# Optimization experiments

Hardware: AMD Instinct MI355X
Metric: run time of the kernel (lower is better)

## Reference

```python
import jax, jax.numpy as jnp
import numpy as np

N = 8192      # nodes (N_features)
D = 64        # oscillator dimension
E_K = 262144  # Kuramoto coupling edges
E_HK = 262144 # Hopfield-Kuramoto coupling edges
H = 64        # interaction MLP hidden width (N_weights)
KAPPA_K = 2.0
KAPPA_H = 2.0


def setup_inputs() -> dict:
    key = jax.random.key(0)
    ks = jax.random.split(key, 9)
    return dict(
        state_H=jax.random.normal(ks[0], (N,), dtype=jnp.float32),
        state_K=jax.random.normal(ks[1], (N, D), dtype=jnp.float32),
        W_H=jax.random.normal(ks[2], (N, N), dtype=jnp.float32) / np.float32(np.sqrt(N)),
        omega=jax.random.normal(ks[3], (D, D), dtype=jnp.float32),
        w1=jax.random.normal(ks[4], (1, H), dtype=jnp.float32),
        b1=jnp.zeros((H,), dtype=jnp.float32),
        w2=jax.random.normal(ks[5], (H, 1), dtype=jnp.float32) / np.float32(np.sqrt(H)),
        ind_K=jax.random.randint(ks[6], (E_K, 2), 0, N),
        ind_HK=jax.random.randint(ks[7], (E_HK, 2), 0, N),
    )


def _interaction_K(s, w1, b1, w2):
    # edgewise scalar MLP: [E] -> [E], dE/ds of the Kuramoto interaction energy
    h = jnp.tanh(s[:, None] @ w1 + b1)  # [E, H]
    return (h @ w2)[:, 0]               # [E]


def reference(state_H, state_K, W_H, omega, w1, b1, w2, ind_K, ind_HK):
    # normalize oscillator states onto unit sphere (per node)
    state_K = state_K / jnp.linalg.norm(state_K, axis=1, keepdims=True)

    i, j = ind_HK[:, 0], ind_HK[:, 1]
    Gram = jnp.sum(state_K[i] * state_K[j], axis=1)  # [E_HK]

    # Hopfield model: g = LNet.get_g(state_H), f_H = Hopfield_model(t, state_H, ...)
    g = jnp.tanh(state_H)                 # [N]
    f_H = -state_H + W_H @ g              # [N] dense Hopfield dynamics
    f_H = f_H.at[i].add(Gram * g[j] / KAPPA_H)
    f_H = f_H.at[j].add(Gram * g[i] / KAPPA_H)

    # Kuramoto edge coupling
    p, q = ind_K[:, 0], ind_K[:, 1]
    s = jnp.sum(state_K[p] * state_K[q], axis=1)        # [E_K]
    dE_ds = _interaction_K(s, w1, b1, w2)[:, None]      # [E_K, 1]
    f_K = jnp.zeros_like(state_K)
    f_K = f_K.at[p].add(dE_ds * state_K[q])
    f_K = f_K.at[q].add(dE_ds * state_K[p])

    # Hopfield->Kuramoto coupling
    G = (g[i] * g[j])[:, None]                          # [E_HK, 1]
    f_K = f_K.at[i].add(-G * state_K[j] / KAPPA_K)
    f_K = f_K.at[j].add(-G * state_K[i] / KAPPA_K)

    # project onto tangent of the sphere + antisymmetric rotation
    f_K = (-f_K
           + state_K * jnp.sum(state_K * f_K, axis=1, keepdims=True)
           + state_K @ ((omega - omega.T) * 0.5))
    return (f_H, f_K)
```

## Files before the change

### kernel.cpp

```cpp
#include <hip/hip_runtime.h>
#include <math.h>

#define N 8192
#define D 64
#define E_K 262144
#define E_HK 262144
#define NEDGE (E_K + E_HK)
#define CAP 256

constexpr float INV_KAPPA = 0.5f;

__device__ inline float fast_tanh(float x) {
  x = fminf(15.f, fmaxf(-15.f, x));
  float e = __expf(2.f * x);
  return (e - 1.f) * __builtin_amdgcn_rcpf(e + 1.f);
}

__device__ inline float wave_reduce(float v) {
  #pragma unroll
  for (int off = 32; off > 0; off >>= 1) v += __shfl_xor(v, off);
  return v;
}

__global__ __launch_bounds__(256) void prep_scatter_kernel(
    const float* __restrict__ state_K, const float* __restrict__ state_H,
    const float* __restrict__ omega,
    const int* __restrict__ ind_HK, const int* __restrict__ ind_K,
    float* __restrict__ Knorm, float* __restrict__ g, float* __restrict__ Om,
    int* __restrict__ cursor, int* __restrict__ entries) {
  int b = blockIdx.x;
  if (b < 2048) {
    int t = b * 256 + threadIdx.x;
    int i, j, bit;
    if (t < E_HK) {
      int2 e = ((const int2*)ind_HK)[t];
      i = e.x; j = e.y; bit = (int)0x80000000;
    } else {
      int2 e = ((const int2*)ind_K)[t - E_HK];
      i = e.x; j = e.y; bit = 0;
    }
    int s0 = atomicAdd(&cursor[i], 1);
    if (s0 < CAP) entries[i * CAP + s0] = j | bit;
    int s1 = atomicAdd(&cursor[j], 1);
    if (s1 < CAP) entries[j * CAP + s1] = i | bit;
  } else if (b < 4096) {
    int lane = threadIdx.x & 63;
    int row  = (b - 2048) * 4 + (threadIdx.x >> 6);
    float v  = state_K[row * D + lane];
    float ss = wave_reduce(v * v);
    Knorm[row * D + lane] = v * __builtin_amdgcn_rcpf(sqrtf(ss));
    if (lane == 0) g[row] = fast_tanh(state_H[row]);
  } else {
    for (int t = threadIdx.x; t < D * D; t += 256) {
      int a = t >> 6, c = t & 63;
      Om[t] = 0.5f * (omega[a * D + c] - omega[c * D + a]);
    }
  }
}

__global__ __launch_bounds__(256) void mega_kernel(
    const float* __restrict__ W_H, const float* __restrict__ state_H,
    const float* __restrict__ Knorm, const float* __restrict__ g,
    const float* __restrict__ Om, const float* __restrict__ w1,
    const float* __restrict__ b1, const float* __restrict__ w2,
    const int* __restrict__ cursor, const int* __restrict__ entries,
    float* __restrict__ f_H, float* __restrict__ f_K) {
  int row  = blockIdx.x;
  int lane = threadIdx.x & 63;
  int wv   = threadIdx.x >> 6;

  const float4* Wrow = reinterpret_cast<const float4*>(W_H + (size_t)row * N);
  float4 wreg[8];
  #pragma unroll
  for (int k = 0; k < 8; ++k) wreg[k] = Wrow[threadIdx.x + k * 256];

  float kr  = Knorm[row * D + lane];
  float gr  = g[row];
  float w1l = w1[lane], b1l = b1[lane], w2l = w2[lane];

  __shared__ int sh_ent[CAP];
  int len = min(cursor[row], CAP);
  for (int e = threadIdx.x; e < len; e += 256)
    sh_ent[e] = entries[row * CAP + e];
  __syncthreads();

  float acc  = 0.f;
  float accH = 0.f;
  for (int e = wv; e < len; e += 4) {
    int ent   = sh_ent[e];
    int other = ent & 0x7FFFFFFF;
    float ko  = Knorm[other * D + lane];
    if (ent < 0) {
      float go = g[other];
      acc  += (-gr * go * INV_KAPPA) * ko;
      accH += go * ko;
    } else {
      float dot = wave_reduce(kr * ko);
      float de  = wave_reduce(fast_tanh(dot * w1l + b1l) * w2l);
      acc += de * ko;
    }
  }

  const float4* g4 = reinterpret_cast<const float4*>(g);
  float mv = 0.f;
  #pragma unroll
  for (int k = 0; k < 8; ++k) {
    float4 gg = g4[threadIdx.x + k * 256];
    mv += wreg[k].x * gg.x + wreg[k].y * gg.y +
          wreg[k].z * gg.z + wreg[k].w * gg.w;
  }
  mv = wave_reduce(mv);

  __shared__ float sAcc[4][D];
  __shared__ float sAccH[4][D];
  __shared__ float sMv[4];
  sAcc[wv][lane]  = acc;
  sAccH[wv][lane] = accH;
  if (lane == 0) sMv[wv] = mv;
  __syncthreads();

  if (wv == 0) {
    float tot  = sAcc[0][lane] + sAcc[1][lane] + sAcc[2][lane] + sAcc[3][lane];
    float totH = sAccH[0][lane] + sAccH[1][lane] + sAccH[2][lane] + sAccH[3][lane];
    float rd = wave_reduce(kr * tot);
    float sh = wave_reduce(kr * totH);
    float krot = 0.f;
    #pragma unroll
    for (int d = 0; d < D; ++d)
      krot += __shfl(kr, d) * Om[d * D + lane];
    f_K[row * D + lane] = -tot + kr * rd + krot;
    if (lane == 0)
      f_H[row] = -state_H[row] + sMv[0] + sMv[1] + sMv[2] + sMv[3]
                 + sh * INV_KAPPA;
  }
}

extern "C" void kernel_launch(void* const* d_in, const int* in_sizes, int n_in,
                              void* d_out, int out_size, void* d_ws, size_t ws_size,
                              hipStream_t stream) {
  const float* state_H = (const float*)d_in[0];
  const float* state_K = (const float*)d_in[1];
  const float* W_H     = (const float*)d_in[2];
  const float* omega   = (const float*)d_in[3];
  const float* w1      = (const float*)d_in[4];
  const float* b1      = (const float*)d_in[5];
  const float* w2      = (const float*)d_in[6];
  const int*   ind_K   = (const int*)d_in[7];
  const int*   ind_HK  = (const int*)d_in[8];

  float* f_H = (float*)d_out;
  float* f_K = (float*)d_out + N;

  char* ws = (char*)d_ws;
  int*   entries = (int*)ws;               ws += (size_t)N * CAP * sizeof(int);
  float* Knorm   = (float*)ws;             ws += (size_t)N * D * sizeof(float);
  float* g       = (float*)ws;             ws += N * sizeof(float);
  float* Om      = (float*)ws;             ws += D * D * sizeof(float);
  int*   cursor  = (int*)ws;

  hipMemsetAsync(cursor, 0, N * sizeof(int), stream);
  prep_scatter_kernel<<<4097, 256, 0, stream>>>(
      state_K, state_H, omega, ind_HK, ind_K, Knorm, g, Om, cursor, entries);
  mega_kernel<<<N, 256, 0, stream>>>(W_H, state_H, Knorm, g, Om, w1, b1, w2,
                                     cursor, entries, f_H, f_K);
}
```

Before: 499.2 us.

## Replace per-edge MLP with interpolated lookup table and batch edge dot reductions

Precomputes the scalar interaction MLP on a 2049-point grid over [-1,1] in the prep kernel and replaces the per-edge tanh MLP plus wave reduction with linear interpolation from a shared-memory table. Edge processing is also batched eight at a time so the neighbor loads and the shuffle reductions of the dot products are interleaved for more memory- and instruction-level parallelism. This removes one wave reduction and a tanh per Kuramoto edge, at the cost of interpolation error in the MLP output. Each block must also load the table into LDS, and register pressure goes up.

```diff
diff --git a/kernel.cpp b/kernel.cpp
--- a/kernel.cpp
+++ b/kernel.cpp
@@ -7,6 +7,8 @@
 #define E_HK 262144
 #define NEDGE (E_K + E_HK)
 #define CAP 256
+#define TAB_N 2048
+#define BATCH 8
 
 constexpr float INV_KAPPA = 0.5f;
 
@@ -26,8 +28,11 @@
     const float* __restrict__ state_K, const float* __restrict__ state_H,
     const float* __restrict__ omega,
     const int* __restrict__ ind_HK, const int* __restrict__ ind_K,
+    const float* __restrict__ w1, const float* __restrict__ b1,
+    const float* __restrict__ w2,
     float* __restrict__ Knorm, float* __restrict__ g, float* __restrict__ Om,
-    int* __restrict__ cursor, int* __restrict__ entries) {
+    float* __restrict__ Tab, int* __restrict__ cursor,
+    int* __restrict__ entries) {
   int b = blockIdx.x;
   if (b < 2048) {
     int t = b * 256 + threadIdx.x;
@@ -50,19 +55,27 @@
     float ss = wave_reduce(v * v);
     Knorm[row * D + lane] = v * __builtin_amdgcn_rcpf(sqrtf(ss));
     if (lane == 0) g[row] = fast_tanh(state_H[row]);
-  } else {
+  } else if (b == 4096) {
     for (int t = threadIdx.x; t < D * D; t += 256) {
       int a = t >> 6, c = t & 63;
       Om[t] = 0.5f * (omega[a * D + c] - omega[c * D + a]);
     }
+  } else {
+    int lane = threadIdx.x & 63;
+    int p = (b - 4097) * 4 + (threadIdx.x >> 6);
+    if (p <= TAB_N) {
+      float s = (float)p * (2.0f / TAB_N) - 1.0f;
+      float t = fast_tanh(s * w1[lane] + b1[lane]) * w2[lane];
+      t = wave_reduce(t);
+      if (lane == 0) Tab[p] = t;
+    }
   }
 }
 
 __global__ __launch_bounds__(256) void mega_kernel(
     const float* __restrict__ W_H, const float* __restrict__ state_H,
     const float* __restrict__ Knorm, const float* __restrict__ g,
-    const float* __restrict__ Om, const float* __restrict__ w1,
-    const float* __restrict__ b1, const float* __restrict__ w2,
+    const float* __restrict__ Om, const float* __restrict__ Tab,
     const int* __restrict__ cursor, const int* __restrict__ entries,
     float* __restrict__ f_H, float* __restrict__ f_K) {
   int row  = blockIdx.x;
@@ -74,30 +87,52 @@
   #pragma unroll
   for (int k = 0; k < 8; ++k) wreg[k] = Wrow[threadIdx.x + k * 256];
 
-  float kr  = Knorm[row * D + lane];
-  float gr  = g[row];
-  float w1l = w1[lane], b1l = b1[lane], w2l = w2[lane];
-
-  __shared__ int sh_ent[CAP];
+  float kr = Knorm[row * D + lane];
+  float gr = g[row];
+
+  __shared__ int   sh_ent[CAP];
+  __shared__ float sTab[TAB_N + 1];
   int len = min(cursor[row], CAP);
   for (int e = threadIdx.x; e < len; e += 256)
     sh_ent[e] = entries[row * CAP + e];
+  for (int t = threadIdx.x; t <= TAB_N; t += 256)
+    sTab[t] = Tab[t];
   __syncthreads();
 
   float acc  = 0.f;
   float accH = 0.f;
-  for (int e = wv; e < len; e += 4) {
-    int ent   = sh_ent[e];
-    int other = ent & 0x7FFFFFFF;
-    float ko  = Knorm[other * D + lane];
-    if (ent < 0) {
-      float go = g[other];
-      acc  += (-gr * go * INV_KAPPA) * ko;
-      accH += go * ko;
-    } else {
-      float dot = wave_reduce(kr * ko);
-      float de  = wave_reduce(fast_tanh(dot * w1l + b1l) * w2l);
-      acc += de * ko;
+  for (int base = wv * BATCH; base < len; base += 4 * BATCH) {
+    int   ents[BATCH];
+    float kov[BATCH], dv[BATCH];
+    #pragma unroll
+    for (int k = 0; k < BATCH; ++k) {
+      if (base + k < len) {
+        ents[k] = sh_ent[base + k];
+        kov[k]  = Knorm[(size_t)(ents[k] & 0x7FFFFFFF) * D + lane];
+      } else { ents[k] = 0; kov[k] = 0.f; }
+    }
+    #pragma unroll
+    for (int k = 0; k < BATCH; ++k) dv[k] = kr * kov[k];
+    #pragma unroll
+    for (int off = 32; off > 0; off >>= 1) {
+      #pragma unroll
+      for (int k = 0; k < BATCH; ++k) dv[k] += __shfl_xor(dv[k], off);
+    }
+    #pragma unroll
+    for (int k = 0; k < BATCH; ++k) {
+      int ent = ents[k];
+      if (ent < 0) {
+        float go = g[ent & 0x7FFFFFFF];
+        acc  += (-gr * go * INV_KAPPA) * kov[k];
+        accH += go * kov[k];
+      } else {
+        float x = fminf(fmaxf((dv[k] + 1.0f) * (TAB_N * 0.5f), 0.0f),
+                        (float)TAB_N);
+        int   i  = min((int)x, TAB_N - 1);
+        float fr = x - (float)i;
+        float de = sTab[i] + (sTab[i + 1] - sTab[i]) * fr;
+        acc += de * kov[k];
+      }
     }
   }
 
@@ -156,11 +191,13 @@
   float* Knorm   = (float*)ws;             ws += (size_t)N * D * sizeof(float);
   float* g       = (float*)ws;             ws += N * sizeof(float);
   float* Om      = (float*)ws;             ws += D * D * sizeof(float);
+  float* Tab     = (float*)ws;             ws += (TAB_N + 1) * sizeof(float);
   int*   cursor  = (int*)ws;
 
   hipMemsetAsync(cursor, 0, N * sizeof(int), stream);
-  prep_scatter_kernel<<<4097, 256, 0, stream>>>(
-      state_K, state_H, omega, ind_HK, ind_K, Knorm, g, Om, cursor, entries);
-  mega_kernel<<<N, 256, 0, stream>>>(W_H, state_H, Knorm, g, Om, w1, b1, w2,
+  prep_scatter_kernel<<<4097 + 513, 256, 0, stream>>>(
+      state_K, state_H, omega, ind_HK, ind_K, w1, b1, w2,
+      Knorm, g, Om, Tab, cursor, entries);
+  mega_kernel<<<N, 256, 0, stream>>>(W_H, state_H, Knorm, g, Om, Tab,
                                      cursor, entries, f_H, f_K);
 }
```

Result: no change. 505.3 us (+1.2%).
